# Kernel tuning notes

Measured on AMD Instinct MI355X. Metric: run time of the kernel, lower is better.

The kernel has to match this reference:

```python
import jax, jax.numpy as jnp
import numpy as np

EMBED_DIM = 1024
HEADS = 16
D_K = EMBED_DIM // HEADS
B, S = 2, 2048


def setup_inputs() -> dict:
    key = jax.random.key(0)
    ks = jax.random.split(key, 8)
    scale = 1.0 / np.sqrt(EMBED_DIM)
    inp = {
        "key": jax.random.normal(ks[0], (B, S, EMBED_DIM), dtype=jnp.float32),
        "query": jax.random.normal(ks[1], (B, S, EMBED_DIM), dtype=jnp.float32),
        "value": jax.random.normal(ks[2], (B, S, EMBED_DIM), dtype=jnp.float32),
        # torch nn.Linear stores weight as [out, in]; y = x @ W.T
        "Wq": jax.random.normal(ks[3], (EMBED_DIM, EMBED_DIM), dtype=jnp.float32) * scale,
        "Wk": jax.random.normal(ks[4], (EMBED_DIM, EMBED_DIM), dtype=jnp.float32) * scale,
        "Wv": jax.random.normal(ks[5], (EMBED_DIM, EMBED_DIM), dtype=jnp.float32) * scale,
        "Wo": jax.random.normal(ks[6], (EMBED_DIM, EMBED_DIM), dtype=jnp.float32) * scale,
        "bo": jax.random.normal(ks[7], (EMBED_DIM,), dtype=jnp.float32) * scale,
        # causal mask, True = keep (matches masked_fill(~mask, -1e20))
        "mask": jnp.tril(jnp.ones((S, S), dtype=jnp.bool_))[None, None, :, :],
    }
    return inp


def _split_heads(x):
    b, s, _ = x.shape
    return x.reshape(b, s, HEADS, D_K).transpose(0, 2, 1, 3)  # [B,H,S,d_k]


def reference(key, query, value, Wq, Wk, Wv, Wo, bo, mask):
    b, q_len = query.shape[0], query.shape[1]
    k = _split_heads(key @ Wk.T)
    q = _split_heads(query @ Wq.T)
    v = _split_heads(value @ Wv.T)
    scores = jnp.einsum('bhqd,bhkd->bhqk', q, k) / np.sqrt(D_K)
    scores = jnp.where(mask, scores, jnp.float32(-1e20))
    attn = jax.nn.softmax(scores, axis=-1)
    out = jnp.einsum('bhqk,bhkd->bhqd', attn, v)
    out = out.transpose(0, 2, 1, 3).reshape(b, q_len, HEADS * D_K)
    return out @ Wo.T + bo
```

## Files before the change

### kernel.cpp

```cpp
#include <hip/hip_runtime.h>
#include <cstdint>
#include <cstddef>


typedef __bf16 bf16;
typedef __bf16 bf16x4 __attribute__((ext_vector_type(4)));
typedef __bf16 bf16x8 __attribute__((ext_vector_type(8)));
typedef float f32x4 __attribute__((ext_vector_type(4)));

#define MFMA(a, b, c) __builtin_amdgcn_mfma_f32_16x16x32_bf16(a, b, c, 0, 0, 0)

constexpr int EMBED = 1024;
constexpr int SEQ = 2048;
constexpr int HEADS = 16;
constexpr int DK = 64;
constexpr int BH = 32;

__device__ __forceinline__ void gl16(const bf16* g, bf16* l) {
  __builtin_amdgcn_global_load_lds(
      (const __attribute__((address_space(1))) unsigned int*)g,
      (__attribute__((address_space(3))) unsigned int*)l, 16, 0, 0);
}

__global__ __launch_bounds__(256) void probe_kernel(const unsigned short* __restrict__ wq,
                                                    int* __restrict__ flag) {
  __shared__ int cnt;
  int t = threadIdx.x;
  if (t == 0) cnt = 0;
  __syncthreads();
  unsigned short u = wq[2 * t];
  int e = (u >> 7) & 0xFF;
  int sane = (e >= 100 && e <= 130) ? 1 : 0;
  atomicAdd(&cnt, sane);
  __syncthreads();
  if (t == 0) flag[0] = (cnt < 128) ? 1 : 0;
}

struct ConvArgs {
  const void* src[8];
  bf16* dst[8];
  int n8[8];
  const int* flag;
};

__global__ __launch_bounds__(256) void convert_kernel(ConvArgs a) {
  const int seg = blockIdx.y;
  const void* s = a.src[seg];
  bf16* d = a.dst[seg];
  const int n8 = a.n8[seg];
  const int isf32 = a.flag[0];
  for (int i = blockIdx.x * 256 + threadIdx.x; i < n8; i += gridDim.x * 256) {
    if (isf32) {
      const float* sp = (const float*)s + (size_t)i * 8;
      float4 x = *(const float4*)sp, y = *(const float4*)(sp + 4);
      bf16x8 v;
      v[0] = (bf16)x.x; v[1] = (bf16)x.y; v[2] = (bf16)x.z; v[3] = (bf16)x.w;
      v[4] = (bf16)y.x; v[5] = (bf16)y.y; v[6] = (bf16)y.z; v[7] = (bf16)y.w;
      *(bf16x8*)(d + (size_t)i * 8) = v;
    } else {
      *(uint4*)(d + (size_t)i * 8) = *(const uint4*)((const bf16*)s + (size_t)i * 8);
    }
  }
}

__device__ __forceinline__ void gemm_body(
    const bf16* __restrict__ X, const bf16* __restrict__ W,
    const bf16* __restrict__ bias, bf16* __restrict__ outb,
    float* __restrict__ outf, int mode, bf16* As, bf16* Bs, int m0, int n0)
{
  const int t = threadIdx.x;
  const int lane = t & 63, wave = t >> 6;
  const int wm = wave >> 1, wn = wave & 1;
  const int l16 = lane & 15, quad = lane >> 4;

  f32x4 acc[4][2] = {};

  for (int k0 = 0; k0 < EMBED; k0 += 64) {
    __syncthreads();
#pragma unroll
    for (int i = 0; i < 4; ++i) {
      int idx = t + i * 256;
      int r = idx >> 3;
      int cl = (idx & 7) ^ (r & 7);
      gl16(X + (size_t)(m0 + r) * EMBED + k0 + cl * 8, As + (wave * 64 + i * 256) * 8);
    }
#pragma unroll
    for (int i = 0; i < 2; ++i) {
      int idx = t + i * 256;
      int r = idx >> 3;
      int cl = (idx & 7) ^ (r & 7);
      gl16(W + (size_t)(n0 + r) * EMBED + k0 + cl * 8, Bs + (wave * 64 + i * 256) * 8);
    }
    __syncthreads();

#pragma unroll
    for (int ks = 0; ks < 2; ++ks) {
      bf16x8 a[4], b[2];
#pragma unroll
      for (int mi = 0; mi < 4; ++mi) {
        int row = wm * 64 + mi * 16 + l16;
        a[mi] = *(const bf16x8*)(As + row * 64 + (((ks * 4 + quad) ^ (row & 7)) * 8));
      }
#pragma unroll
      for (int ni = 0; ni < 2; ++ni) {
        int row = wn * 32 + ni * 16 + l16;
        b[ni] = *(const bf16x8*)(Bs + row * 64 + (((ks * 4 + quad) ^ (row & 7)) * 8));
      }
#pragma unroll
      for (int mi = 0; mi < 4; ++mi)
#pragma unroll
        for (int ni = 0; ni < 2; ++ni)
          acc[mi][ni] = MFMA(a[mi], b[ni], acc[mi][ni]);
    }
  }

#pragma unroll
  for (int mi = 0; mi < 4; ++mi) {
#pragma unroll
    for (int ni = 0; ni < 2; ++ni) {
      int n = n0 + wn * 32 + ni * 16 + l16;
#pragma unroll
      for (int r = 0; r < 4; ++r) {
        int m = m0 + wm * 64 + mi * 16 + quad * 4 + r;
        float v = acc[mi][ni][r];
        if (mode == 2) {
          outf[(size_t)m * EMBED + n] = v + (float)bias[n];
        } else {
          int b_ = m >> 11, s = m & (SEQ - 1);
          int h = n >> 6, d = n & 63;
          int bh = b_ * HEADS + h;
          if (mode == 0)
            outb[((size_t)bh * SEQ + s) * DK + d] = (bf16)v;
          else
            outb[((size_t)bh * DK + d) * SEQ + s] = (bf16)v;
        }
      }
    }
  }
}

struct QkvArgs {
  const bf16 *X0, *X1, *X2;
  const bf16 *W0, *W1, *W2;
  bf16 *O0, *O1, *O2;
};

__global__ __launch_bounds__(256) void qkv_gemm(QkvArgs args) {
  __shared__ alignas(16) bf16 As[128 * 64];
  __shared__ alignas(16) bf16 Bs[64 * 64];
  const int z = blockIdx.z;
  const bf16* X = (z == 0) ? args.X0 : (z == 1) ? args.X1 : args.X2;
  const bf16* W = (z == 0) ? args.W0 : (z == 1) ? args.W1 : args.W2;
  bf16* O      = (z == 0) ? args.O0 : (z == 1) ? args.O1 : args.O2;
  int mode = (z == 2) ? 1 : 0;
  gemm_body(X, W, nullptr, O, nullptr, mode, As, Bs,
            blockIdx.x * 128, blockIdx.y * 64);
}

__global__ __launch_bounds__(256) void out_gemm(const bf16* __restrict__ X,
                                               const bf16* __restrict__ W,
                                               const bf16* __restrict__ bias,
                                               float* __restrict__ out) {
  __shared__ alignas(16) bf16 As[128 * 64];
  __shared__ alignas(16) bf16 Bs[64 * 64];
  gemm_body(X, W, bias, nullptr, out, 2, As, Bs,
            blockIdx.x * 128, blockIdx.y * 64);
}

__global__ __launch_bounds__(512, 4) void attn_kernel(
    const bf16* __restrict__ qbuf, const bf16* __restrict__ kbuf,
    const bf16* __restrict__ vtbuf, bf16* __restrict__ ctx)
{
  __shared__ alignas(16) bf16 Ks[2][64 * 64];
  __shared__ alignas(16) bf16 VTs[2][64 * 64];
  __shared__ alignas(16) bf16 Ps[128 * 72];

  const int t = threadIdx.x;
  const int g = (blockIdx.x + blockIdx.y) & 15;
  const int qt = (blockIdx.y & 16) ? (15 - g) : g;
  const int bh = blockIdx.y;
  const int q0 = qt * 128;
  const int lane = t & 63, w = t >> 6;
  const int l16 = lane & 15, quad = lane >> 4;

  const bf16* Kp0 = kbuf + (size_t)bh * SEQ * DK;
  const bf16* Vp0 = vtbuf + (size_t)bh * DK * SEQ;

  const int sr = t >> 3;
  const int scl = (t & 7) ^ (sr & 7);

  gl16(Kp0 + (size_t)sr * DK + scl * 8, &Ks[0][0] + w * 512);
  gl16(Vp0 + (size_t)sr * SEQ + scl * 8, &VTs[0][0] + w * 512);

  const bf16* Qg = qbuf + ((size_t)bh * SEQ + q0 + w * 16 + l16) * DK;
  bf16x8 qf[2];
  qf[0] = *(const bf16x8*)(Qg + quad * 8);
  qf[1] = *(const bf16x8*)(Qg + 32 + quad * 8);

  asm volatile("s_waitcnt vmcnt(0)");
  __builtin_amdgcn_s_barrier();
  __builtin_amdgcn_sched_barrier(0);

  const int qglob = q0 + w * 16 + l16;
  float lst = 0.f;
  f32x4 o[4] = {};
  bf16* Pw = Ps + w * 16 * 72;

  constexpr float SC = 0.125f * 1.44269504f;
  constexpr float BI = -8.0f * 1.44269504f;

  const int ktmax = 2 * qt + 1;
  for (int kt = 0; kt <= ktmax; ++kt) {
    const int c = kt & 1;
    const bf16* Kc = &Ks[c][0];
    const bf16* Vc = &VTs[c][0];

    if (kt < ktmax) {
      const bf16* Kg = Kp0 + ((size_t)(kt + 1) * 64 + sr) * DK;
      const bf16* Vg = Vp0 + (size_t)sr * SEQ + (kt + 1) * 64;
      gl16(Kg + scl * 8, &Ks[c ^ 1][0] + w * 512);
      gl16(Vg + scl * 8, &VTs[c ^ 1][0] + w * 512);
    }

    f32x4 sacc[4] = {};
#pragma unroll
    for (int ks = 0; ks < 2; ++ks) {
#pragma unroll
      for (int mi = 0; mi < 4; ++mi) {
        int row = mi * 16 + l16;
        bf16x8 kf = *(const bf16x8*)(Kc + row * 64 + (((ks * 4 + quad) ^ (row & 7)) * 8));
        sacc[mi] = MFMA(kf, qf[ks], sacc[mi]);
      }
    }

    const bool need_mask = (kt * 64 + 63 > q0 + w * 16);
    float ls = 0.f;
    const int kbase = kt * 64 + quad * 4;
#pragma unroll
    for (int mi = 0; mi < 4; ++mi) {
      bf16x4 pv;
#pragma unroll
      for (int r = 0; r < 4; ++r) {
        float arg = __builtin_fmaf(sacc[mi][r], SC, BI);
        if (need_mask && (kbase + mi * 16 + r > qglob)) arg = -1e30f;
        float p = __builtin_exp2f(arg);
        ls += p;
        pv[r] = (bf16)p;
      }
      *(bf16x4*)(Pw + l16 * 72 + mi * 16 + quad * 4) = pv;
    }
    ls += __shfl_xor(ls, 16);
    ls += __shfl_xor(ls, 32);
    lst += ls;

#pragma unroll
    for (int ks = 0; ks < 2; ++ks) {
      bf16x8 pf = *(const bf16x8*)(Pw + l16 * 72 + ks * 32 + quad * 8);
#pragma unroll
      for (int dt = 0; dt < 4; ++dt) {
        int row = dt * 16 + l16;
        bf16x8 vf = *(const bf16x8*)(Vc + row * 64 +
                                     (((ks * 4 + quad) ^ (row & 7)) * 8));
        o[dt] = MFMA(vf, pf, o[dt]);
      }
    }

    asm volatile("s_waitcnt vmcnt(0)");
    __builtin_amdgcn_s_barrier();
    __builtin_amdgcn_sched_barrier(0);
  }

  const float inv = 1.0f / lst;
  const int b_ = bh >> 4, h = bh & 15;
  bf16* dst = ctx + ((size_t)b_ * SEQ + qglob) * EMBED + h * DK;
#pragma unroll
  for (int dt = 0; dt < 4; ++dt) {
    bf16x4 v;
#pragma unroll
    for (int r = 0; r < 4; ++r) v[r] = (bf16)(o[dt][r] * inv);
    *(bf16x4*)(dst + dt * 16 + quad * 4) = v;
  }
}

extern "C" void kernel_launch(void* const* d_in, const int* in_sizes, int n_in,
                              void* d_out, int out_size, void* d_ws, size_t ws_size,
                              hipStream_t stream) {
  const void* key   = d_in[0];
  const void* query = d_in[1];
  const void* value = d_in[2];
  const void* Wq    = d_in[3];
  const void* Wk    = d_in[4];
  const void* Wv    = d_in[5];
  const void* Wo    = d_in[6];
  const void* bo    = d_in[7];
  float* out = (float*)d_out;

  int* flag = (int*)d_ws;
  char* base = (char*)d_ws + 256;
  const size_t XN = (size_t)2 * SEQ * EMBED;
  const size_t WN = (size_t)EMBED * EMBED;
  const size_t per = (size_t)BH * SEQ * DK;

  bf16* cq  = (bf16*)base;
  bf16* ck  = cq + XN;
  bf16* cv  = ck + XN;
  bf16* cWq = cv + XN;
  bf16* cWk = cWq + WN;
  bf16* cWv = cWk + WN;
  bf16* cWo = cWv + WN;
  bf16* cbo = cWo + WN;
  bf16* qb  = cbo + 1024;
  bf16* kb  = qb + per;
  bf16* vtb = kb + per;
  bf16* ctx = vtb + per;

  probe_kernel<<<1, 256, 0, stream>>>((const unsigned short*)Wq, flag);

  ConvArgs ca;
  ca.src[0] = query; ca.dst[0] = cq;  ca.n8[0] = (int)(XN / 8);
  ca.src[1] = key;   ca.dst[1] = ck;  ca.n8[1] = (int)(XN / 8);
  ca.src[2] = value; ca.dst[2] = cv;  ca.n8[2] = (int)(XN / 8);
  ca.src[3] = Wq;    ca.dst[3] = cWq; ca.n8[3] = (int)(WN / 8);
  ca.src[4] = Wk;    ca.dst[4] = cWk; ca.n8[4] = (int)(WN / 8);
  ca.src[5] = Wv;    ca.dst[5] = cWv; ca.n8[5] = (int)(WN / 8);
  ca.src[6] = Wo;    ca.dst[6] = cWo; ca.n8[6] = (int)(WN / 8);
  ca.src[7] = bo;    ca.dst[7] = cbo; ca.n8[7] = 128;
  ca.flag = flag;
  convert_kernel<<<dim3(2048, 8), 256, 0, stream>>>(ca);

  QkvArgs qa{cq, ck, cv, cWq, cWk, cWv, qb, kb, vtb};
  qkv_gemm<<<dim3(32, 16, 3), 256, 0, stream>>>(qa);
  attn_kernel<<<dim3(16, 32), 512, 0, stream>>>(qb, kb, vtb, ctx);
  out_gemm<<<dim3(32, 16), 256, 0, stream>>>(ctx, cWo, cbo, out);
}
```

Baseline: 238.8 us.

## Software-pipeline attention: triple-buffer K/V and overlap next QK^T with softmax

Moves the K/V shared-memory ring from two stages to three and prefetches tiles two iterations ahead. Computes the next tile's QK^T MFMAs while the current tile's exp2/softmax runs, so matrix and vector work interleave. Raises wave priority around the PV MFMA block. The cost is more LDS (roughly 16KB extra) and more live registers for the snext accumulators, which could cut occupancy under launch_bounds(512,4).

Result: faster. 234.0 us (-2.0%).

```diff
diff --git a/kernel.cpp b/kernel.cpp
--- a/kernel.cpp
+++ b/kernel.cpp
@@ -171,8 +171,8 @@
     const bf16* __restrict__ qbuf, const bf16* __restrict__ kbuf,
     const bf16* __restrict__ vtbuf, bf16* __restrict__ ctx)
 {
-  __shared__ alignas(16) bf16 Ks[2][64 * 64];
-  __shared__ alignas(16) bf16 VTs[2][64 * 64];
+  __shared__ alignas(16) bf16 Ks[3][64 * 64];
+  __shared__ alignas(16) bf16 VTs[3][64 * 64];
   __shared__ alignas(16) bf16 Ps[128 * 72];
 
   const int t = threadIdx.x;
@@ -188,18 +188,35 @@
 
   const int sr = t >> 3;
   const int scl = (t & 7) ^ (sr & 7);
-
-  gl16(Kp0 + (size_t)sr * DK + scl * 8, &Ks[0][0] + w * 512);
-  gl16(Vp0 + (size_t)sr * SEQ + scl * 8, &VTs[0][0] + w * 512);
+  const size_t kgoff = (size_t)sr * DK + scl * 8;
+  const size_t vgoff = (size_t)sr * SEQ + scl * 8;
 
   const bf16* Qg = qbuf + ((size_t)bh * SEQ + q0 + w * 16 + l16) * DK;
   bf16x8 qf[2];
   qf[0] = *(const bf16x8*)(Qg + quad * 8);
   qf[1] = *(const bf16x8*)(Qg + 32 + quad * 8);
 
+  const int ktmax = 2 * qt + 1;
+
+  gl16(Kp0 + kgoff, &Ks[0][0] + w * 512);
+  gl16(Vp0 + vgoff, &VTs[0][0] + w * 512);
+  gl16(Kp0 + (size_t)64 * DK + kgoff, &Ks[1][0] + w * 512);
+  gl16(Vp0 + 64 + vgoff, &VTs[1][0] + w * 512);
+
   asm volatile("s_waitcnt vmcnt(0)");
   __builtin_amdgcn_s_barrier();
   __builtin_amdgcn_sched_barrier(0);
+
+  f32x4 scur[4];
+#pragma unroll
+  for (int mi = 0; mi < 4; ++mi) {
+    int row = mi * 16 + l16;
+    bf16x8 k0 = *(const bf16x8*)(&Ks[0][0] + row * 64 + ((quad ^ (row & 7)) * 8));
+    bf16x8 k1 = *(const bf16x8*)(&Ks[0][0] + row * 64 + (((4 + quad) ^ (row & 7)) * 8));
+    f32x4 z = {};
+    z = MFMA(k0, qf[0], z);
+    scur[mi] = MFMA(k1, qf[1], z);
+  }
 
   const int qglob = q0 + w * 16 + l16;
   float lst = 0.f;
@@ -209,39 +226,35 @@
   constexpr float SC = 0.125f * 1.44269504f;
   constexpr float BI = -8.0f * 1.44269504f;
 
-  const int ktmax = 2 * qt + 1;
+  int c_cur = 0, c_next = 1, c_stage = 2;
+
   for (int kt = 0; kt <= ktmax; ++kt) {
-    const int c = kt & 1;
-    const bf16* Kc = &Ks[c][0];
-    const bf16* Vc = &VTs[c][0];
-
-    if (kt < ktmax) {
-      const bf16* Kg = Kp0 + ((size_t)(kt + 1) * 64 + sr) * DK;
-      const bf16* Vg = Vp0 + (size_t)sr * SEQ + (kt + 1) * 64;
-      gl16(Kg + scl * 8, &Ks[c ^ 1][0] + w * 512);
-      gl16(Vg + scl * 8, &VTs[c ^ 1][0] + w * 512);
-    }
-
-    f32x4 sacc[4] = {};
-#pragma unroll
-    for (int ks = 0; ks < 2; ++ks) {
-#pragma unroll
-      for (int mi = 0; mi < 4; ++mi) {
+    if (kt + 2 <= ktmax) {
+      gl16(Kp0 + (size_t)(kt + 2) * 64 * DK + kgoff, &Ks[c_stage][0] + w * 512);
+      gl16(Vp0 + (size_t)(kt + 2) * 64 + vgoff, &VTs[c_stage][0] + w * 512);
+    }
+
+    const bool has_next = (kt < ktmax);
+    const bf16* Kn = &Ks[c_next][0];
+    const bool need_mask = (kt * 64 + 63 > q0 + w * 16);
+    const int kbase = kt * 64 + quad * 4;
+    float ls = 0.f;
+    f32x4 snext[4];
+
+#pragma unroll
+    for (int mi = 0; mi < 4; ++mi) {
+      if (has_next) {
         int row = mi * 16 + l16;
-        bf16x8 kf = *(const bf16x8*)(Kc + row * 64 + (((ks * 4 + quad) ^ (row & 7)) * 8));
-        sacc[mi] = MFMA(kf, qf[ks], sacc[mi]);
-      }
-    }
-
-    const bool need_mask = (kt * 64 + 63 > q0 + w * 16);
-    float ls = 0.f;
-    const int kbase = kt * 64 + quad * 4;
-#pragma unroll
-    for (int mi = 0; mi < 4; ++mi) {
+        bf16x8 k0 = *(const bf16x8*)(Kn + row * 64 + ((quad ^ (row & 7)) * 8));
+        bf16x8 k1 = *(const bf16x8*)(Kn + row * 64 + (((4 + quad) ^ (row & 7)) * 8));
+        f32x4 z = {};
+        z = MFMA(k0, qf[0], z);
+        snext[mi] = MFMA(k1, qf[1], z);
+      }
       bf16x4 pv;
 #pragma unroll
       for (int r = 0; r < 4; ++r) {
-        float arg = __builtin_fmaf(sacc[mi][r], SC, BI);
+        float arg = __builtin_fmaf(scur[mi][r], SC, BI);
         if (need_mask && (kbase + mi * 16 + r > qglob)) arg = -1e30f;
         float p = __builtin_exp2f(arg);
         ls += p;
@@ -253,6 +266,8 @@
     ls += __shfl_xor(ls, 32);
     lst += ls;
 
+    const bf16* Vc = &VTs[c_cur][0];
+    __builtin_amdgcn_s_setprio(1);
 #pragma unroll
     for (int ks = 0; ks < 2; ++ks) {
       bf16x8 pf = *(const bf16x8*)(Pw + l16 * 72 + ks * 32 + quad * 8);
@@ -264,10 +279,17 @@
         o[dt] = MFMA(vf, pf, o[dt]);
       }
     }
+    __builtin_amdgcn_s_setprio(0);
 
     asm volatile("s_waitcnt vmcnt(0)");
     __builtin_amdgcn_s_barrier();
     __builtin_amdgcn_sched_barrier(0);
+
+    if (has_next) {
+#pragma unroll
+      for (int mi = 0; mi < 4; ++mi) scur[mi] = snext[mi];
+    }
+    int tmp = c_cur; c_cur = c_next; c_next = c_stage; c_stage = tmp;
   }
 
   const float inv = 1.0f / lst;
```
